# Performance work log

Hardware: AMD Instinct MI355X
Metric: run time of the kernel (lower is better)

Reference implementation:

```python
import jax, jax.numpy as jnp
import numpy as np

B = 512
DIM_X = 128
DIM_Y = 128
HIDDEN = 512


def setup_inputs() -> dict:
    key = jax.random.key(0)
    kx, ky, kw1, kw2 = jax.random.split(key, 4)
    x = jax.random.normal(kx, (B, DIM_X), dtype=jnp.float32)
    y = jax.random.normal(ky, (B, DIM_Y), dtype=jnp.float32)
    # Glorot-ish scaling for the Dense layers
    W1 = jax.random.normal(kw1, (DIM_X + DIM_Y, HIDDEN), dtype=jnp.float32) * (1.0 / np.sqrt(DIM_X + DIM_Y))
    b1 = jnp.zeros((HIDDEN,), dtype=jnp.float32)
    W2 = jax.random.normal(kw2, (HIDDEN, 1), dtype=jnp.float32) * (1.0 / np.sqrt(HIDDEN))
    b2 = jnp.zeros((1,), dtype=jnp.float32)
    return {"x": x, "y": y, "W1": W1, "b1": b1, "W2": W2, "b2": b2}


def reference(x, y, W1, b1, W2, b2):
    # scores[i, j] = f(concat(x_i, y_j)) with f = Dense(512, relu) -> Dense(1).
    # Since the first Dense is linear in the concatenated input, split W1 into
    # the x-block and y-block and broadcast-sum instead of materializing the
    # [B*B, dim_x+dim_y] concat tensor (same math as tile+concat+matmul).
    dim_x = x.shape[1]
    hx = x @ W1[:dim_x]          # [B, H]
    hy = y @ W1[dim_x:]          # [B, H]
    h = jax.nn.relu(hx[:, None, :] + hy[None, :, :] + b1)  # [B, B, H]
    scores = jnp.einsum('ijh,h->ij', h, W2[:, 0]) + b2[0]   # [B, B]
    return scores
```

## Files before the change

kernel.cpp:

```cpp
#include <hip/hip_runtime.h>


#define BATCH 512
#define DX    128
#define HID   512

typedef _Float16 half2_t __attribute__((ext_vector_type(2)));

static __device__ __forceinline__ half2_t u2h(unsigned int u) {
    union { unsigned int u; half2_t h; } c; c.u = u; return c.h;
}
static __device__ __forceinline__ unsigned int h2u(half2_t h) {
    union { half2_t h; unsigned int u; } c; c.h = h; return c.u;
}

__global__ __launch_bounds__(256) void proj_kernel(
    const float* __restrict__ x, const float* __restrict__ y,
    const float* __restrict__ W1, const float* __restrict__ b1,
    _Float16* __restrict__ hxy)
{
    const int part = blockIdx.y;
    const int row0 = blockIdx.x * 8;
    const int h    = blockIdx.z * 256 + threadIdx.x;
    const float* __restrict__ src = part ? y : x;
    const float* __restrict__ W   = W1 + part * DX * HID;

    __shared__ float s[8][DX];
    {
        const int t = threadIdx.x;
        const int r = t >> 5, c4 = (t & 31) << 2;
        const float4 v = *(const float4*)&src[(row0 + r) * DX + c4];
        s[r][c4] = v.x; s[r][c4 + 1] = v.y; s[r][c4 + 2] = v.z; s[r][c4 + 3] = v.w;
    }
    __syncthreads();

    float acc[8] = {0.f, 0.f, 0.f, 0.f, 0.f, 0.f, 0.f, 0.f};
    #pragma unroll 8
    for (int k = 0; k < DX; ++k) {
        const float w = W[k * HID + h];
        #pragma unroll
        for (int r = 0; r < 8; ++r) acc[r] = fmaf(s[r][k], w, acc[r]);
    }
    const float bias = part ? b1[h] : 0.0f;
    #pragma unroll
    for (int r = 0; r < 8; ++r)
        hxy[(part * BATCH + row0 + r) * HID + h] = (_Float16)(acc[r] + bias);
}

#define TI   128
#define TJ   64
#define HPW  32
#define ST   33

__global__ __launch_bounds__(512, 2) void score_kernel(
    const _Float16* __restrict__ hxy, const float* __restrict__ W2,
    unsigned int* __restrict__ pws16)
{
    __shared__ unsigned int sA[TI * ST];
    __shared__ unsigned int sB[TJ * ST];
    __shared__ unsigned int sW[HPW];

    const int i0  = blockIdx.y * TI;
    const int j0  = blockIdx.x * TJ;
    const int z   = blockIdx.z;
    const int hp0 = z * HPW;
    const int tid = threadIdx.x;
    const unsigned int* __restrict__ hx32 = (const unsigned int*)hxy;

    #pragma unroll
    for (int it = 0; it < 2; ++it) {
        const int s = tid + it * 512;
        const int row = s >> 3, q = s & 7;
        const uint4 v = *(const uint4*)&hx32[(i0 + row) * 256 + hp0 + (q << 2)];
        unsigned int* p = &sA[row * ST + (q << 2)];
        p[0] = v.x; p[1] = v.y; p[2] = v.z; p[3] = v.w;
    }
    {
        const int row = tid >> 3, q = tid & 7;
        const uint4 v = *(const uint4*)&hx32[(BATCH + j0 + row) * 256 + hp0 + (q << 2)];
        unsigned int* p = &sB[row * ST + (q << 2)];
        p[0] = v.x; p[1] = v.y; p[2] = v.z; p[3] = v.w;
    }
    if (tid < HPW) {
        const float2 w = *(const float2*)&W2[2 * (hp0 + tid)];
        half2_t wh; wh.x = (_Float16)w.x; wh.y = (_Float16)w.y;
        sW[tid] = h2u(wh);
    }
    __syncthreads();

    const int tx = tid & 15;
    const int ty = tid >> 4;
    const unsigned int* pa = &sA[(ty << 2) * ST];
    const unsigned int* pb = &sB[(tx << 2) * ST];

    float acc[4][4] = {{0.f,0.f,0.f,0.f},{0.f,0.f,0.f,0.f},
                       {0.f,0.f,0.f,0.f},{0.f,0.f,0.f,0.f}};
    const half2_t hz = {(_Float16)0, (_Float16)0};

    #pragma unroll 4
    for (int hp = 0; hp < HPW; ++hp) {
        const half2_t w = u2h(sW[hp]);
        half2_t a[4], bb[4];
        #pragma unroll
        for (int r = 0; r < 4; ++r) a[r]  = u2h(pa[r * ST + hp]);
        #pragma unroll
        for (int c = 0; c < 4; ++c) bb[c] = u2h(pb[c * ST + hp]);
        #pragma unroll
        for (int r = 0; r < 4; ++r)
            #pragma unroll
            for (int c = 0; c < 4; ++c) {
                half2_t t = a[r] + bb[c];
                t = __builtin_elementwise_max(t, hz);
                acc[r][c] = __builtin_amdgcn_fdot2(t, w, acc[r][c], false);
            }
    }

    const int i = i0 + (ty << 2);
    unsigned int* dst = pws16 + z * (BATCH * BATCH / 2);
    #pragma unroll
    for (int r = 0; r < 4; ++r) {
        half2_t p0, p1;
        p0.x = (_Float16)acc[r][0]; p0.y = (_Float16)acc[r][1];
        p1.x = (_Float16)acc[r][2]; p1.y = (_Float16)acc[r][3];
        uint2 st; st.x = h2u(p0); st.y = h2u(p1);
        *(uint2*)&dst[(i + r) * (BATCH / 2) + (j0 >> 1) + (tx << 1)] = st;
    }
}

__global__ __launch_bounds__(256) void reduce_kernel(
    const unsigned int* __restrict__ pws16, const float* __restrict__ b2,
    float* __restrict__ out)
{
    const int gid = blockIdx.x * 256 + threadIdx.x;
    float s0 = 0.f, s1 = 0.f;
    #pragma unroll
    for (int zz = 0; zz < 8; ++zz) {
        const half2_t v = u2h(pws16[zz * (BATCH * BATCH / 2) + gid]);
        s0 += (float)v.x; s1 += (float)v.y;
    }
    const float bs = b2[0];
    *(float2*)&out[gid * 2] = make_float2(s0 + bs, s1 + bs);
}

extern "C" void kernel_launch(void* const* d_in, const int* in_sizes, int n_in,
                              void* d_out, int out_size, void* d_ws, size_t ws_size,
                              hipStream_t stream) {
    const float* x  = (const float*)d_in[0];
    const float* y  = (const float*)d_in[1];
    const float* W1 = (const float*)d_in[2];
    const float* b1 = (const float*)d_in[3];
    const float* W2 = (const float*)d_in[4];
    const float* b2 = (const float*)d_in[5];
    float* out = (float*)d_out;

    _Float16* hxy       = (_Float16*)d_ws;
    unsigned int* pws16 = (unsigned int*)((char*)d_ws + (1 << 20));

    proj_kernel<<<dim3(BATCH / 8, 2, 2), 256, 0, stream>>>(x, y, W1, b1, hxy);
    score_kernel<<<dim3(BATCH / TJ, BATCH / TI, 8), 512, 0, stream>>>(hxy, W2, pws16);
    reduce_kernel<<<dim3(BATCH * BATCH / 2 / 256), 256, 0, stream>>>(pws16, b2, out);
}
```

Measured before the change: 84.68 us.

## Replace split-H partial buffer and reduce kernel with atomic accumulation into output

Removes the separate reduce kernel and the fp16 partial-sum workspace. The projection kernel now also fills the output with b2, and each score block atomically adds its fp32 partial scores into the output. The shared-memory layout is transposed so each thread loads its four A and four B values with one 128-bit LDS read. The projection kernel is also vectorized to process four hidden columns and two rows per thread. This saves one launch and the workspace round trip, but adds eight-way atomic contention per output element and makes the summation order nondeterministic.

Result: slower. 110.7 us (+30.7%).

```diff
diff --git a/kernel.cpp b/kernel.cpp
--- a/kernel.cpp
+++ b/kernel.cpp
@@ -17,69 +17,105 @@
 __global__ __launch_bounds__(256) void proj_kernel(
     const float* __restrict__ x, const float* __restrict__ y,
     const float* __restrict__ W1, const float* __restrict__ b1,
-    _Float16* __restrict__ hxy)
+    const float* __restrict__ b2,
+    _Float16* __restrict__ hxy, float* __restrict__ out)
 {
     const int part = blockIdx.y;
+    if (part == 2) {
+        const float bs = b2[0];
+        const int gid = (blockIdx.z * 64 + blockIdx.x) * 256 + threadIdx.x;
+        const float4 v = make_float4(bs, bs, bs, bs);
+        float4* o4 = (float4*)out;
+        o4[gid] = v;
+        o4[gid + 32768] = v;
+        return;
+    }
+
     const int row0 = blockIdx.x * 8;
-    const int h    = blockIdx.z * 256 + threadIdx.x;
+    const int h0   = blockIdx.z * 256;
     const float* __restrict__ src = part ? y : x;
     const float* __restrict__ W   = W1 + part * DX * HID;
 
-    __shared__ float s[8][DX];
+    __shared__ __align__(16) float s[8][DX];
     {
         const int t = threadIdx.x;
         const int r = t >> 5, c4 = (t & 31) << 2;
-        const float4 v = *(const float4*)&src[(row0 + r) * DX + c4];
-        s[r][c4] = v.x; s[r][c4 + 1] = v.y; s[r][c4 + 2] = v.z; s[r][c4 + 3] = v.w;
+        *(float4*)&s[r][c4] = *(const float4*)&src[(row0 + r) * DX + c4];
     }
     __syncthreads();
 
-    float acc[8] = {0.f, 0.f, 0.f, 0.f, 0.f, 0.f, 0.f, 0.f};
-    #pragma unroll 8
-    for (int k = 0; k < DX; ++k) {
-        const float w = W[k * HID + h];
+    const int hthr = threadIdx.x & 63;
+    const int rg   = threadIdx.x >> 6;
+    const int h    = h0 + hthr * 4;
+    const int ra   = rg * 2, rb = ra + 1;
+
+    float a0 = 0.f, a1 = 0.f, a2 = 0.f, a3 = 0.f;
+    float c0 = 0.f, c1 = 0.f, c2 = 0.f, c3 = 0.f;
+
+    #pragma unroll 2
+    for (int k4 = 0; k4 < DX / 4; ++k4) {
+        const float4 xa = *(const float4*)&s[ra][k4 * 4];
+        const float4 xb = *(const float4*)&s[rb][k4 * 4];
         #pragma unroll
-        for (int r = 0; r < 8; ++r) acc[r] = fmaf(s[r][k], w, acc[r]);
+        for (int kk = 0; kk < 4; ++kk) {
+            const float4 wv = *(const float4*)&W[(k4 * 4 + kk) * HID + h];
+            const float fa = (kk == 0) ? xa.x : (kk == 1) ? xa.y : (kk == 2) ? xa.z : xa.w;
+            const float fb = (kk == 0) ? xb.x : (kk == 1) ? xb.y : (kk == 2) ? xb.z : xb.w;
+            a0 = fmaf(fa, wv.x, a0); a1 = fmaf(fa, wv.y, a1);
+            a2 = fmaf(fa, wv.z, a2); a3 = fmaf(fa, wv.w, a3);
+            c0 = fmaf(fb, wv.x, c0); c1 = fmaf(fb, wv.y, c1);
+            c2 = fmaf(fb, wv.z, c2); c3 = fmaf(fb, wv.w, c3);
+        }
     }
-    const float bias = part ? b1[h] : 0.0f;
-    #pragma unroll
-    for (int r = 0; r < 8; ++r)
-        hxy[(part * BATCH + row0 + r) * HID + h] = (_Float16)(acc[r] + bias);
+
+    float4 bias = make_float4(0.f, 0.f, 0.f, 0.f);
+    if (part) bias = *(const float4*)&b1[h];
+
+    half2_t p0, p1;
+    p0.x = (_Float16)(a0 + bias.x); p0.y = (_Float16)(a1 + bias.y);
+    p1.x = (_Float16)(a2 + bias.z); p1.y = (_Float16)(a3 + bias.w);
+    uint2 st0; st0.x = h2u(p0); st0.y = h2u(p1);
+    *(uint2*)&hxy[(part * BATCH + row0 + ra) * HID + h] = st0;
+
+    p0.x = (_Float16)(c0 + bias.x); p0.y = (_Float16)(c1 + bias.y);
+    p1.x = (_Float16)(c2 + bias.z); p1.y = (_Float16)(c3 + bias.w);
+    uint2 st1; st1.x = h2u(p0); st1.y = h2u(p1);
+    *(uint2*)&hxy[(part * BATCH + row0 + rb) * HID + h] = st1;
 }
 
 #define TI   128
 #define TJ   64
 #define HPW  32
-#define ST   33
+#define IST  132
+#define JST  68
 
 __global__ __launch_bounds__(512, 2) void score_kernel(
     const _Float16* __restrict__ hxy, const float* __restrict__ W2,
-    unsigned int* __restrict__ pws16)
+    float* __restrict__ out)
 {
-    __shared__ unsigned int sA[TI * ST];
-    __shared__ unsigned int sB[TJ * ST];
+    __shared__ __align__(16) unsigned int sA[HPW * IST];
+    __shared__ __align__(16) unsigned int sB[HPW * JST];
     __shared__ unsigned int sW[HPW];
 
     const int i0  = blockIdx.y * TI;
     const int j0  = blockIdx.x * TJ;
-    const int z   = blockIdx.z;
-    const int hp0 = z * HPW;
+    const int hp0 = blockIdx.z * HPW;
     const int tid = threadIdx.x;
     const unsigned int* __restrict__ hx32 = (const unsigned int*)hxy;
 
     #pragma unroll
     for (int it = 0; it < 2; ++it) {
-        const int s = tid + it * 512;
-        const int row = s >> 3, q = s & 7;
+        const int sidx = tid + it * 512;
+        const int row = sidx >> 3, q = sidx & 7;
         const uint4 v = *(const uint4*)&hx32[(i0 + row) * 256 + hp0 + (q << 2)];
-        unsigned int* p = &sA[row * ST + (q << 2)];
-        p[0] = v.x; p[1] = v.y; p[2] = v.z; p[3] = v.w;
+        unsigned int* p = &sA[(q << 2) * IST + row];
+        p[0 * IST] = v.x; p[1 * IST] = v.y; p[2 * IST] = v.z; p[3 * IST] = v.w;
     }
     {
         const int row = tid >> 3, q = tid & 7;
         const uint4 v = *(const uint4*)&hx32[(BATCH + j0 + row) * 256 + hp0 + (q << 2)];
-        unsigned int* p = &sB[row * ST + (q << 2)];
-        p[0] = v.x; p[1] = v.y; p[2] = v.z; p[3] = v.w;
+        unsigned int* p = &sB[(q << 2) * JST + row];
+        p[0 * JST] = v.x; p[1 * JST] = v.y; p[2 * JST] = v.z; p[3 * JST] = v.w;
     }
     if (tid < HPW) {
         const float2 w = *(const float2*)&W2[2 * (hp0 + tid)];
@@ -90,8 +126,8 @@
 
     const int tx = tid & 15;
     const int ty = tid >> 4;
-    const unsigned int* pa = &sA[(ty << 2) * ST];
-    const unsigned int* pb = &sB[(tx << 2) * ST];
+    const unsigned int* pa = &sA[ty << 2];
+    const unsigned int* pb = &sB[tx << 2];
 
     float acc[4][4] = {{0.f,0.f,0.f,0.f},{0.f,0.f,0.f,0.f},
                        {0.f,0.f,0.f,0.f},{0.f,0.f,0.f,0.f}};
@@ -100,46 +136,29 @@
     #pragma unroll 4
     for (int hp = 0; hp < HPW; ++hp) {
         const half2_t w = u2h(sW[hp]);
-        half2_t a[4], bb[4];
-        #pragma unroll
-        for (int r = 0; r < 4; ++r) a[r]  = u2h(pa[r * ST + hp]);
-        #pragma unroll
-        for (int c = 0; c < 4; ++c) bb[c] = u2h(pb[c * ST + hp]);
+        const uint4 av = *(const uint4*)&pa[hp * IST];
+        const uint4 bv = *(const uint4*)&pb[hp * JST];
+        half2_t a[4] = {u2h(av.x), u2h(av.y), u2h(av.z), u2h(av.w)};
+        half2_t b[4] = {u2h(bv.x), u2h(bv.y), u2h(bv.z), u2h(bv.w)};
         #pragma unroll
         for (int r = 0; r < 4; ++r)
             #pragma unroll
             for (int c = 0; c < 4; ++c) {
-                half2_t t = a[r] + bb[c];
+                half2_t t = a[r] + b[c];
                 t = __builtin_elementwise_max(t, hz);
                 acc[r][c] = __builtin_amdgcn_fdot2(t, w, acc[r][c], false);
             }
     }
 
-    const int i = i0 + (ty << 2);
-    unsigned int* dst = pws16 + z * (BATCH * BATCH / 2);
+    const int ibase = i0 + (ty << 2);
+    const int jbase = j0 + (tx << 2);
     #pragma unroll
     for (int r = 0; r < 4; ++r) {
-        half2_t p0, p1;
-        p0.x = (_Float16)acc[r][0]; p0.y = (_Float16)acc[r][1];
-        p1.x = (_Float16)acc[r][2]; p1.y = (_Float16)acc[r][3];
-        uint2 st; st.x = h2u(p0); st.y = h2u(p1);
-        *(uint2*)&dst[(i + r) * (BATCH / 2) + (j0 >> 1) + (tx << 1)] = st;
+        float* orow = &out[(ibase + r) * BATCH + jbase];
+        #pragma unroll
+        for (int c = 0; c < 4; ++c)
+            unsafeAtomicAdd(&orow[c], acc[r][c]);
     }
-}
-
-__global__ __launch_bounds__(256) void reduce_kernel(
-    const unsigned int* __restrict__ pws16, const float* __restrict__ b2,
-    float* __restrict__ out)
-{
-    const int gid = blockIdx.x * 256 + threadIdx.x;
-    float s0 = 0.f, s1 = 0.f;
-    #pragma unroll
-    for (int zz = 0; zz < 8; ++zz) {
-        const half2_t v = u2h(pws16[zz * (BATCH * BATCH / 2) + gid]);
-        s0 += (float)v.x; s1 += (float)v.y;
-    }
-    const float bs = b2[0];
-    *(float2*)&out[gid * 2] = make_float2(s0 + bs, s1 + bs);
 }
 
 extern "C" void kernel_launch(void* const* d_in, const int* in_sizes, int n_in,
@@ -153,10 +172,8 @@
     const float* b2 = (const float*)d_in[5];
     float* out = (float*)d_out;
 
-    _Float16* hxy       = (_Float16*)d_ws;
-    unsigned int* pws16 = (unsigned int*)((char*)d_ws + (1 << 20));
+    _Float16* hxy = (_Float16*)d_ws;
 
-    proj_kernel<<<dim3(BATCH / 8, 2, 2), 256, 0, stream>>>(x, y, W1, b1, hxy);
-    score_kernel<<<dim3(BATCH / TJ, BATCH / TI, 8), 512, 0, stream>>>(hxy, W2, pws16);
-    reduce_kernel<<<dim3(BATCH * BATCH / 2 / 256), 256, 0, stream>>>(pws16, b2, out);
+    proj_kernel<<<dim3(64, 3, 2), 256, 0, stream>>>(x, y, W1, b1, b2, hxy, out);
+    score_kernel<<<dim3(8, 4, 8), 512, 0, stream>>>(hxy, W2, out);
 }
```
